# Kernel tuning notes

Measured on AMD Instinct MI355X. Metric: run time of the kernel, lower is better.

## Reference

```python
import jax, jax.numpy as jnp
import numpy as np

DIM = 1024
NUM_HEADS = 16
HEAD_DIM = DIM // NUM_HEADS
EPS = 1e-6


def layer_norm(x, gamma, beta):
    # normalize over last dim (head_dim)
    mu = jnp.mean(x, axis=-1, keepdims=True)
    var = jnp.mean(jnp.square(x - mu), axis=-1, keepdims=True)
    return (x - mu) / jnp.sqrt(var + EPS) * gamma + beta


def apply_rope(q, k):
    # q, k: [B, S, H, D]; computed in fp32 (attn_fp32=True)
    seq_len, head_dim = q.shape[1], q.shape[3]
    half = head_dim // 2
    freq_range = jnp.arange(half, dtype=jnp.float32) / half
    inv_freq = 1.0 / (10000.0 ** freq_range)                       # [half]
    t = jnp.arange(seq_len, dtype=jnp.float32)                     # [S]
    freqs = jnp.outer(t, inv_freq)                                 # [S, half]
    emb = jnp.concatenate([freqs, freqs], axis=-1)                 # [S, D]
    cos = jnp.cos(emb)[None, :, None, :]                           # [1, S, 1, D]
    sin = jnp.sin(emb)[None, :, None, :]

    def rotate_half(x):
        x1, x2 = x[..., :half], x[..., half:]
        return jnp.concatenate([-x2, x1], axis=-1)

    return q * cos + rotate_half(q) * sin, k * cos + rotate_half(k) * sin


def setup_inputs() -> dict:
    key = jax.random.key(0)
    ks = jax.random.split(key, 4)
    B, S = 2, 2048
    x = jax.random.normal(ks[0], (B, S, DIM), dtype=jnp.float32)
    # xavier-uniform-ish scale for linear weights (torch Linear layout: [out, in])
    lim_qkv = float(np.sqrt(6.0 / (DIM + 3 * DIM)))
    w_qkv = jax.random.uniform(ks[1], (3 * DIM, DIM), dtype=jnp.float32, minval=-lim_qkv, maxval=lim_qkv)
    lim_p = float(np.sqrt(6.0 / (DIM + DIM)))
    w_proj = jax.random.uniform(ks[2], (DIM, DIM), dtype=jnp.float32, minval=-lim_p, maxval=lim_p)
    b_proj = jnp.zeros((DIM,), dtype=jnp.float32)
    q_gamma = jnp.ones((HEAD_DIM,), dtype=jnp.float32)
    q_beta = jnp.zeros((HEAD_DIM,), dtype=jnp.float32)
    k_gamma = jnp.ones((HEAD_DIM,), dtype=jnp.float32)
    k_beta = jnp.zeros((HEAD_DIM,), dtype=jnp.float32)
    return {"x": x, "w_qkv": w_qkv, "w_proj": w_proj, "b_proj": b_proj,
            "q_gamma": q_gamma, "q_beta": q_beta, "k_gamma": k_gamma, "k_beta": k_beta}


def reference(x, w_qkv, w_proj, b_proj, q_gamma, q_beta, k_gamma, k_beta):
    B, S, C = x.shape
    H, D = NUM_HEADS, HEAD_DIM
    qkv = jnp.einsum('bsc,oc->bso', x, w_qkv).reshape(B, S, 3, H, D)
    q = layer_norm(qkv[:, :, 0], q_gamma, q_beta)   # [B, S, H, D]
    k = layer_norm(qkv[:, :, 1], k_gamma, k_beta)
    v = qkv[:, :, 2]
    q, k = apply_rope(q, k)
    # attn_fp32=True: scores in fp32
    scale = D ** (-0.5)
    q = q.astype(jnp.float32) * scale
    k = k.astype(jnp.float32)
    v = v.astype(jnp.float32)
    attn = jnp.einsum('bqhd,bkhd->bhqk', q, k)      # [B, H, S, S]
    attn = jax.nn.softmax(attn, axis=-1)
    out = jnp.einsum('bhqk,bkhd->bqhd', attn, v).reshape(B, S, C)
    out = jnp.einsum('bsc,oc->bso', out, w_proj) + b_proj
    return out
```

## Files before the change

### kernel.cpp

```cpp
#include <hip/hip_runtime.h>
#include <math.h>

#define DIM   1024
#define NH    16
#define HD    64
#define BATCH 2
#define SEQ   2048
#define EPS   1e-6f

typedef __attribute__((ext_vector_type(8))) short bf16x8;
typedef __attribute__((ext_vector_type(4))) float f32x4;

#define EXP2F(x) __builtin_amdgcn_exp2f(x)
#define LOG2E 1.4426950408889634f
#define SOFTMAX_SHIFT 12.0f

__device__ __forceinline__ float bf2f(unsigned short u) {
  return __uint_as_float(((unsigned int)u) << 16);
}
__device__ __forceinline__ unsigned short f2bf(float f) {
  unsigned int u = __float_as_uint(f);
  unsigned int r = (u + 0x7FFFu + ((u >> 16) & 1u)) >> 16;
  return (unsigned short)r;
}
__device__ __forceinline__ unsigned int pack_bf16_trunc(float p0, float p1) {
  return (__float_as_uint(p1) & 0xFFFF0000u) | (__float_as_uint(p0) >> 16);
}

__device__ __forceinline__ void async_copy16(const void* g, void* l) {
  __builtin_amdgcn_global_load_lds(
      (const __attribute__((address_space(1))) unsigned int*)g,
      (__attribute__((address_space(3))) unsigned int*)l, 16, 0, 0);
}


__global__ void detect_dtype(const unsigned short* __restrict__ w, int* __restrict__ flag) {
  __shared__ int cnt;
  if (threadIdx.x == 0) cnt = 0;
  __syncthreads();
  int c = 0;
  for (int i = threadIdx.x; i < 4096; i += 256) {
    unsigned short u = w[i];
    if ((u & 0x7F80u) >= 0x3F80u) ++c;
  }
  atomicAdd(&cnt, c);
  __syncthreads();
  if (threadIdx.x == 0) *flag = (cnt >= 64) ? 1 : 0;
}

__global__ __launch_bounds__(256)
void rope_table(float2* __restrict__ tab) {
  const int idx = blockIdx.x * 256 + threadIdx.x;
  const int s = idx >> 5, f = idx & 31;
  const float invf = expf(-((float)f * (1.f / 32.f)) * 9.210340371976184f);
  float sn, cs;
  sincosf((float)s * invf, &sn, &cs);
  tab[idx] = make_float2(cs, sn);
}

__global__ __launch_bounds__(256)
void convert_bf16(const void* __restrict__ src, unsigned short* __restrict__ dst,
                  int n, const int* __restrict__ flagp) {
  const bool isf32 = (*flagp != 0);
  const int i = (blockIdx.x * 256 + threadIdx.x) * 8;
  if (i >= n) return;
  if (isf32) {
    const float* s = (const float*)src + i;
    float4 a = *(const float4*)s;
    float4 b = *(const float4*)(s + 4);
    ushort4 lo, hi;
    lo.x = f2bf(a.x); lo.y = f2bf(a.y); lo.z = f2bf(a.z); lo.w = f2bf(a.w);
    hi.x = f2bf(b.x); hi.y = f2bf(b.y); hi.z = f2bf(b.z); hi.w = f2bf(b.w);
    *(ushort4*)&dst[i] = lo;
    *(ushort4*)&dst[i + 4] = hi;
  } else {
    *(uint4*)&dst[i] = *(const uint4*)((const unsigned short*)src + i);
  }
}

__device__ __forceinline__ float ld_param(const void* p, bool isf32, int idx) {
  return isf32 ? ((const float*)p)[idx] : bf2f(((const unsigned short*)p)[idx]);
}

__global__ __launch_bounds__(256)
void gemm_qkv(const unsigned short* __restrict__ A, const unsigned short* __restrict__ B,
              unsigned short* __restrict__ Qb, unsigned short* __restrict__ Kb,
              unsigned short* __restrict__ VbT,
              const void* __restrict__ qg, const void* __restrict__ qbe,
              const void* __restrict__ kg, const void* __restrict__ kbe,
              const float2* __restrict__ tab, const int* __restrict__ flagp) {
  __shared__ __attribute__((aligned(16))) unsigned short As[128 * 32];
  __shared__ __attribute__((aligned(16))) unsigned short Bs[128 * 32];

  const int K = DIM;
  const int tid  = threadIdx.x;
  const int wv   = tid >> 6;
  const int lane = tid & 63;
  const int l15  = lane & 15;
  const int quad = lane >> 4;
  const int wm = wv >> 1, wn = wv & 1;
  const int bm = blockIdx.y * 128;
  const int bn = blockIdx.x * 128;
  const int qsw = (quad ^ ((l15 >> 1) & 3)) * 8;

  f32x4 acc[4][4];
#pragma unroll
  for (int i = 0; i < 4; ++i)
#pragma unroll
    for (int j = 0; j < 4; ++j) acc[i][j] = (f32x4){0.f, 0.f, 0.f, 0.f};

  const int srow = tid >> 2;
  const int kseg = (((tid & 3) ^ ((tid >> 3) & 3))) * 8;
  const unsigned short* Ag = A + (size_t)(bm + srow) * K + kseg;
  const unsigned short* Bg = B + (size_t)(bn + srow) * K + kseg;
  unsigned short* AsW = &As[wv * 512];
  unsigned short* BsW = &Bs[wv * 512];

  for (int k0 = 0; k0 < K; k0 += 32) {
    __syncthreads();
    async_copy16(Ag + k0, AsW);
    async_copy16(Ag + (size_t)64 * K + k0, AsW + 2048);
    async_copy16(Bg + k0, BsW);
    async_copy16(Bg + (size_t)64 * K + k0, BsW + 2048);
    __syncthreads();

    bf16x8 af[4], bf[4];
#pragma unroll
    for (int mt = 0; mt < 4; ++mt)
      af[mt] = *(const bf16x8*)&As[(wm * 64 + mt * 16 + l15) * 32 + qsw];
#pragma unroll
    for (int nt = 0; nt < 4; ++nt)
      bf[nt] = *(const bf16x8*)&Bs[(wn * 64 + nt * 16 + l15) * 32 + qsw];
#pragma unroll
    for (int mt = 0; mt < 4; ++mt)
#pragma unroll
      for (int nt = 0; nt < 4; ++nt)
        acc[mt][nt] = __builtin_amdgcn_mfma_f32_16x16x32_bf16(af[mt], bf[nt], acc[mt][nt], 0, 0, 0);
  }

  const bool isf32 = (*flagp != 0);
  const int type = bn >> 10;
  const int h = ((bn & 1023) >> 6) + wn;

  if (type == 2) {
#pragma unroll
    for (int mt = 0; mt < 4; ++mt) {
      const int r0 = bm + wm * 64 + mt * 16 + quad * 4;
      const int b = r0 >> 11, s0 = r0 & 2047;
#pragma unroll
      for (int nt = 0; nt < 4; ++nt) {
        const int d = nt * 16 + l15;
        uint2 pk;
        pk.x = ((unsigned int)f2bf(acc[mt][nt][1]) << 16) | f2bf(acc[mt][nt][0]);
        pk.y = ((unsigned int)f2bf(acc[mt][nt][3]) << 16) | f2bf(acc[mt][nt][2]);
        *(uint2*)&VbT[((size_t)(b * NH + h) * HD + d) * SEQ + s0] = pk;
      }
    }
    return;
  }

  unsigned short* plane = (type == 0) ? Qb : Kb;
  const void* gp = (type == 0) ? qg : kg;
  const void* bp = (type == 0) ? qbe : kbe;
  float gam[4], bet[4];
#pragma unroll
  for (int nt = 0; nt < 4; ++nt) {
    gam[nt] = ld_param(gp, isf32, nt * 16 + l15);
    bet[nt] = ld_param(bp, isf32, nt * 16 + l15);
  }
  const float scale = (type == 0) ? (0.125f * LOG2E) : 1.f;

#pragma unroll
  for (int mt = 0; mt < 4; ++mt)
#pragma unroll
    for (int rr = 0; rr < 4; ++rr) {
      const int r = bm + wm * 64 + mt * 16 + quad * 4 + rr;
      const int b = r >> 11, s = r & 2047;
      float sum = acc[mt][0][rr] + acc[mt][1][rr] + acc[mt][2][rr] + acc[mt][3][rr];
      sum += __shfl_xor(sum, 1); sum += __shfl_xor(sum, 2);
      sum += __shfl_xor(sum, 4); sum += __shfl_xor(sum, 8);
      const float mu = sum * (1.f / 64.f);
      float vs = 0.f;
#pragma unroll
      for (int nt = 0; nt < 4; ++nt) {
        const float d = acc[mt][nt][rr] - mu;
        vs += d * d;
      }
      vs += __shfl_xor(vs, 1); vs += __shfl_xor(vs, 2);
      vs += __shfl_xor(vs, 4); vs += __shfl_xor(vs, 8);
      const float rs = rsqrtf(vs * (1.f / 64.f) + EPS);
      float xn[4];
#pragma unroll
      for (int nt = 0; nt < 4; ++nt)
        xn[nt] = (acc[mt][nt][rr] - mu) * rs * gam[nt] + bet[nt];
      const float2 t0 = tab[s * 32 + l15];
      const float2 t1 = tab[s * 32 + 16 + l15];
      float ro[4];
      ro[0] = xn[0] * t0.x - xn[2] * t0.y;
      ro[2] = xn[2] * t0.x + xn[0] * t0.y;
      ro[1] = xn[1] * t1.x - xn[3] * t1.y;
      ro[3] = xn[3] * t1.x + xn[1] * t1.y;
      unsigned short* row = plane + (((size_t)(b * NH + h) * SEQ + s) * HD);
#pragma unroll
      for (int nt = 0; nt < 4; ++nt)
        row[nt * 16 + l15] = f2bf(ro[nt] * scale);
    }
}

#define KIDX(g,k0,key,dim) (((((g)*2+(k0))*64+(key))*32)+(dim))
#define VOFF 8192
#define POFF 16384
#define PIDX(w,row,col) (POFF + ((w)*32+(row))*72 + (col))

__global__ __launch_bounds__(512, 4)
void attn_mfma5(const unsigned short* __restrict__ Qb, const unsigned short* __restrict__ Kb,
                const unsigned short* __restrict__ VbT, unsigned short* __restrict__ O) {
  __shared__ __attribute__((aligned(16))) unsigned short SMEM[34816];

  const int tid  = threadIdx.x;
  const int wv   = tid >> 6;
  const int g    = wv >> 2;
  const int qsub = wv & 3;
  const int lane = tid & 63;
  const int l15  = lane & 15;
  const int quad = lane >> 4;
  const int bh = blockIdx.y;
  const int q0 = blockIdx.x * 128;
  const size_t base  = (size_t)bh * (SEQ * HD);
  const size_t baseT = (size_t)bh * (HD * SEQ);
  const int qsw = (quad ^ ((l15 >> 1) & 3)) * 8;

  bf16x8 qf[2][2];
#pragma unroll
  for (int mt = 0; mt < 2; ++mt)
#pragma unroll
    for (int k0 = 0; k0 < 2; ++k0)
      qf[mt][k0] = *(const bf16x8*)&Qb[base + (size_t)(q0 + qsub * 32 + mt * 16 + l15) * HD + k0 * 32 + quad * 8];

  bf16x8 ones;
#pragma unroll
  for (int j = 0; j < 8; ++j) ones[j] = (short)0x3F80;

  f32x4 oaccT[4][2];
  f32x4 ol[2];
#pragma unroll
  for (int nb = 0; nb < 4; ++nb)
#pragma unroll
    for (int mt = 0; mt < 2; ++mt) oaccT[nb][mt] = (f32x4){0.f, 0.f, 0.f, 0.f};
  ol[0] = (f32x4){0.f, 0.f, 0.f, 0.f};
  ol[1] = (f32x4){0.f, 0.f, 0.f, 0.f};

  const int sseg = (((lane & 3) ^ ((lane >> 3) & 3))) * 8;
  const unsigned short* srcK = Kb + base + (size_t)(qsub * 16 + (lane >> 2)) * HD + sseg;
  const unsigned short* srcV = VbT + baseT + (size_t)(qsub * 16 + (lane >> 2)) * SEQ + sseg;
  unsigned short* dstK0 = &SMEM[KIDX(g, 0, qsub * 16, 0)];
  unsigned short* dstK1 = &SMEM[KIDX(g, 1, qsub * 16, 0)];
  unsigned short* dstV0 = &SMEM[VOFF + KIDX(g, 0, qsub * 16, 0)];
  unsigned short* dstV1 = &SMEM[VOFF + KIDX(g, 1, qsub * 16, 0)];

  for (int it = 0; it < SEQ / 128; ++it) {
    const int kt = it * 128 + g * 64;
    __syncthreads();
    async_copy16(srcK + (size_t)kt * HD,      dstK0);
    async_copy16(srcK + (size_t)kt * HD + 32, dstK1);
    async_copy16(srcV + kt,                   dstV0);
    async_copy16(srcV + kt + 32,              dstV1);
    __syncthreads();

    f32x4 st[4][2];
#pragma unroll
    for (int nb = 0; nb < 4; ++nb)
#pragma unroll
      for (int mt = 0; mt < 2; ++mt) st[nb][mt] = (f32x4){0.f, 0.f, 0.f, 0.f};
#pragma unroll
    for (int k0 = 0; k0 < 2; ++k0)
#pragma unroll
      for (int nb = 0; nb < 4; ++nb) {
        bf16x8 kf = *(const bf16x8*)&SMEM[KIDX(g, k0, nb * 16 + l15, qsw)];
#pragma unroll
        for (int mt = 0; mt < 2; ++mt)
          st[nb][mt] = __builtin_amdgcn_mfma_f32_16x16x32_bf16(kf, qf[mt][k0], st[nb][mt], 0, 0, 0);
      }

#pragma unroll
    for (int mt = 0; mt < 2; ++mt)
#pragma unroll
      for (int nb = 0; nb < 4; ++nb) {
        const float p0 = EXP2F(st[nb][mt][0] - SOFTMAX_SHIFT);
        const float p1 = EXP2F(st[nb][mt][1] - SOFTMAX_SHIFT);
        const float p2 = EXP2F(st[nb][mt][2] - SOFTMAX_SHIFT);
        const float p3 = EXP2F(st[nb][mt][3] - SOFTMAX_SHIFT);
        uint2 pk;
        pk.x = pack_bf16_trunc(p0, p1);
        pk.y = pack_bf16_trunc(p2, p3);
        *(uint2*)&SMEM[PIDX(wv, mt * 16 + l15, nb * 16 + quad * 4)] = pk;
      }

#pragma unroll
    for (int k0 = 0; k0 < 2; ++k0) {
      bf16x8 pf0 = *(const bf16x8*)&SMEM[PIDX(wv, 0 * 16 + l15, k0 * 32 + quad * 8)];
      bf16x8 pf1 = *(const bf16x8*)&SMEM[PIDX(wv, 1 * 16 + l15, k0 * 32 + quad * 8)];
      ol[0] = __builtin_amdgcn_mfma_f32_16x16x32_bf16(ones, pf0, ol[0], 0, 0, 0);
      ol[1] = __builtin_amdgcn_mfma_f32_16x16x32_bf16(ones, pf1, ol[1], 0, 0, 0);
#pragma unroll
      for (int nb = 0; nb < 4; ++nb) {
        bf16x8 vf = *(const bf16x8*)&SMEM[VOFF + KIDX(g, k0, nb * 16 + l15, qsw)];
        oaccT[nb][0] = __builtin_amdgcn_mfma_f32_16x16x32_bf16(vf, pf0, oaccT[nb][0], 0, 0, 0);
        oaccT[nb][1] = __builtin_amdgcn_mfma_f32_16x16x32_bf16(vf, pf1, oaccT[nb][1], 0, 0, 0);
      }
    }
  }

  __syncthreads();
  f32x4* MO = (f32x4*)SMEM;
  float* ML = (float*)(SMEM + POFF);
  if (g == 1) {
#pragma unroll
    for (int mt = 0; mt < 2; ++mt) {
#pragma unroll
      for (int nb = 0; nb < 4; ++nb)
        MO[(((qsub * 2 + mt) * 4 + nb) << 6) + lane] = oaccT[nb][mt];
      if (quad == 0)
        ML[(qsub * 2 + mt) * 16 + l15] = ol[mt][0];
    }
  }
  __syncthreads();
  if (g == 0) {
    const int b = bh >> 4, h = bh & 15;
#pragma unroll
    for (int mt = 0; mt < 2; ++mt) {
      const float l1 = ML[(qsub * 2 + mt) * 16 + l15];
      const float inv = 1.f / (ol[mt][0] + l1);
      const int qrow = q0 + qsub * 32 + mt * 16 + l15;
      unsigned short* orow = O + ((size_t)(b * SEQ + qrow)) * DIM + h * HD;
#pragma unroll
      for (int nb = 0; nb < 4; ++nb) {
        f32x4 o1 = MO[(((qsub * 2 + mt) * 4 + nb) << 6) + lane];
        uint2 pk;
        pk.x = ((unsigned int)f2bf((oaccT[nb][mt][1] + o1[1]) * inv) << 16) |
               f2bf((oaccT[nb][mt][0] + o1[0]) * inv);
        pk.y = ((unsigned int)f2bf((oaccT[nb][mt][3] + o1[3]) * inv) << 16) |
               f2bf((oaccT[nb][mt][2] + o1[2]) * inv);
        *(uint2*)&orow[nb * 16 + quad * 4] = pk;
      }
    }
  }
}

__global__ __launch_bounds__(256)
void gemm_out(const unsigned short* __restrict__ A, const unsigned short* __restrict__ B,
              const void* __restrict__ biasv, void* __restrict__ Cv,
              int M, int N, int K, const int* __restrict__ flagp) {
  __shared__ __attribute__((aligned(16))) unsigned short As[128 * 32];
  __shared__ __attribute__((aligned(16))) unsigned short Bs[64 * 32];

  const int tid  = threadIdx.x;
  const int wv   = tid >> 6;
  const int lane = tid & 63;
  const int l15  = lane & 15;
  const int quad = lane >> 4;
  const int wm = wv >> 1, wn = wv & 1;
  const int bm = blockIdx.y * 128;
  const int bn = blockIdx.x * 64;
  const int qsw = (quad ^ ((l15 >> 1) & 3)) * 8;

  f32x4 acc[4][2];
#pragma unroll
  for (int i = 0; i < 4; ++i)
#pragma unroll
    for (int j = 0; j < 2; ++j) acc[i][j] = (f32x4){0.f, 0.f, 0.f, 0.f};

  const int srow = tid >> 2;
  const int kseg = (((tid & 3) ^ ((tid >> 3) & 3))) * 8;
  const unsigned short* Ag = A + (size_t)(bm + srow) * K + kseg;
  const unsigned short* Bg = B + (size_t)(bn + srow) * K + kseg;
  unsigned short* AsW = &As[wv * 512];
  unsigned short* BsW = &Bs[wv * 512];

  for (int k0 = 0; k0 < K; k0 += 32) {
    __syncthreads();
    async_copy16(Ag + k0, AsW);
    async_copy16(Ag + (size_t)64 * K + k0, AsW + 2048);
    async_copy16(Bg + k0, BsW);
    __syncthreads();

    bf16x8 af[4], bf[2];
#pragma unroll
    for (int mt = 0; mt < 4; ++mt)
      af[mt] = *(const bf16x8*)&As[(wm * 64 + mt * 16 + l15) * 32 + qsw];
#pragma unroll
    for (int nt = 0; nt < 2; ++nt)
      bf[nt] = *(const bf16x8*)&Bs[(wn * 32 + nt * 16 + l15) * 32 + qsw];
#pragma unroll
    for (int mt = 0; mt < 4; ++mt)
#pragma unroll
      for (int nt = 0; nt < 2; ++nt)
        acc[mt][nt] = __builtin_amdgcn_mfma_f32_16x16x32_bf16(af[mt], bf[nt], acc[mt][nt], 0, 0, 0);
  }

  const bool isf32 = (*flagp != 0);
#pragma unroll
  for (int mt = 0; mt < 4; ++mt)
#pragma unroll
    for (int rr = 0; rr < 4; ++rr) {
      const int r = bm + wm * 64 + mt * 16 + quad * 4 + rr;
#pragma unroll
      for (int nt = 0; nt < 2; ++nt) {
        const int c = bn + wn * 32 + nt * 16 + l15;
        const float bias_c = isf32 ? ((const float*)biasv)[c]
                                   : bf2f(((const unsigned short*)biasv)[c]);
        const float o = acc[mt][nt][rr] + bias_c;
        if (isf32) ((float*)Cv)[(size_t)r * N + c] = o;
        else       ((unsigned short*)Cv)[(size_t)r * N + c] = f2bf(o);
      }
    }
}

extern "C" void kernel_launch(void* const* d_in, const int* in_sizes, int n_in,
                              void* d_out, int out_size, void* d_ws, size_t ws_size,
                              hipStream_t stream) {
  const void* x      = d_in[0];
  const void* w_qkv  = d_in[1];
  const void* w_proj = d_in[2];
  const void* b_proj = d_in[3];
  const void* q_g    = d_in[4];
  const void* q_b    = d_in[5];
  const void* k_g    = d_in[6];
  const void* k_b    = d_in[7];

  const size_t PLANE = (size_t)BATCH * NH * SEQ * HD;
  const int NX = BATCH * SEQ * DIM;
  const int NWQ = 3 * DIM * DIM;
  const int NWP = DIM * DIM;

  unsigned short* Qb  = (unsigned short*)d_ws;
  unsigned short* Kb  = Qb + PLANE;
  unsigned short* VbT = Kb + PLANE;
  unsigned short* xb  = VbT + PLANE;
  unsigned short* wqb = xb + PLANE;
  unsigned short* wpb = wqb + NWQ;
  float2* tab = (float2*)(wpb + NWP);
  int* flag = (int*)(tab + SEQ * 32);

  hipLaunchKernelGGL(detect_dtype, dim3(1), dim3(256), 0, stream,
                     (const unsigned short*)w_qkv, flag);
  hipLaunchKernelGGL(rope_table, dim3(SEQ * 32 / 256), dim3(256), 0, stream, tab);

  hipLaunchKernelGGL(convert_bf16, dim3(NX / 8 / 256), dim3(256), 0, stream,
                     x, xb, NX, flag);
  hipLaunchKernelGGL(convert_bf16, dim3(NWQ / 8 / 256), dim3(256), 0, stream,
                     w_qkv, wqb, NWQ, flag);
  hipLaunchKernelGGL(convert_bf16, dim3(NWP / 8 / 256), dim3(256), 0, stream,
                     w_proj, wpb, NWP, flag);

  {
    dim3 grid((3 * DIM) / 128, (BATCH * SEQ) / 128);
    hipLaunchKernelGGL(gemm_qkv, grid, dim3(256), 0, stream,
                       xb, wqb, Qb, Kb, VbT, q_g, q_b, k_g, k_b, tab, flag);
  }
  {
    dim3 grid(SEQ / 128, BATCH * NH);
    hipLaunchKernelGGL(attn_mfma5, grid, dim3(512), 0, stream,
                       Qb, Kb, VbT, xb);
  }
  {
    dim3 grid(DIM / 64, (BATCH * SEQ) / 128);
    hipLaunchKernelGGL(gemm_out, grid, dim3(256), 0, stream,
                       xb, wpb, b_proj, d_out, BATCH * SEQ, DIM, DIM, flag);
  }
}
```

Before: 220.1 us.

## Double-buffer LDS tiles in GEMMs and merge three conversion launches into one

Both GEMM kernels (QKV and output projection) now keep two LDS buffers. The next K-tile's async copies are issued before the MFMAs on the current tile, and one barrier per iteration replaces the previous two, so global loads overlap with compute. Separately, the three bf16 conversion launches are merged into a single kernel that picks its source and destination from the flat index, saving two launches. The cost is double the LDS use in the GEMMs, which may lower occupancy. Whether the asynchronous copies have actually landed before the barrier depends on how async_copy16 waits.

```diff
diff --git a/kernel.cpp b/kernel.cpp
--- a/kernel.cpp
+++ b/kernel.cpp
@@ -7,6 +7,10 @@
 #define BATCH 2
 #define SEQ   2048
 #define EPS   1e-6f
+
+#define NX  (BATCH * SEQ * DIM)
+#define NWQ (3 * DIM * DIM)
+#define NWP (DIM * DIM)
 
 typedef __attribute__((ext_vector_type(8))) short bf16x8;
 typedef __attribute__((ext_vector_type(4))) float f32x4;
@@ -59,11 +63,18 @@
 }
 
 __global__ __launch_bounds__(256)
-void convert_bf16(const void* __restrict__ src, unsigned short* __restrict__ dst,
-                  int n, const int* __restrict__ flagp) {
+void convert_all(const void* __restrict__ x, const void* __restrict__ wq,
+                 const void* __restrict__ wp,
+                 unsigned short* __restrict__ xb, unsigned short* __restrict__ wqb,
+                 unsigned short* __restrict__ wpb, const int* __restrict__ flagp) {
   const bool isf32 = (*flagp != 0);
-  const int i = (blockIdx.x * 256 + threadIdx.x) * 8;
-  if (i >= n) return;
+  int i = (blockIdx.x * 256 + threadIdx.x) * 8;
+  const void* src;
+  unsigned short* dst;
+  if (i < NX) { src = x; dst = xb; }
+  else if (i < NX + NWQ) { src = wq; dst = wqb; i -= NX; }
+  else if (i < NX + NWQ + NWP) { src = wp; dst = wpb; i -= NX + NWQ; }
+  else return;
   if (isf32) {
     const float* s = (const float*)src + i;
     float4 a = *(const float4*)s;
@@ -89,8 +100,8 @@
               const void* __restrict__ qg, const void* __restrict__ qbe,
               const void* __restrict__ kg, const void* __restrict__ kbe,
               const float2* __restrict__ tab, const int* __restrict__ flagp) {
-  __shared__ __attribute__((aligned(16))) unsigned short As[128 * 32];
-  __shared__ __attribute__((aligned(16))) unsigned short Bs[128 * 32];
+  __shared__ __attribute__((aligned(16))) unsigned short As[2][128 * 32];
+  __shared__ __attribute__((aligned(16))) unsigned short Bs[2][128 * 32];
 
   const int K = DIM;
   const int tid  = threadIdx.x;
@@ -113,29 +124,35 @@
   const int kseg = (((tid & 3) ^ ((tid >> 3) & 3))) * 8;
   const unsigned short* Ag = A + (size_t)(bm + srow) * K + kseg;
   const unsigned short* Bg = B + (size_t)(bn + srow) * K + kseg;
-  unsigned short* AsW = &As[wv * 512];
-  unsigned short* BsW = &Bs[wv * 512];
+
+  async_copy16(Ag, &As[0][wv * 512]);
+  async_copy16(Ag + (size_t)64 * K, &As[0][wv * 512 + 2048]);
+  async_copy16(Bg, &Bs[0][wv * 512]);
+  async_copy16(Bg + (size_t)64 * K, &Bs[0][wv * 512 + 2048]);
+  __syncthreads();
 
   for (int k0 = 0; k0 < K; k0 += 32) {
-    __syncthreads();
-    async_copy16(Ag + k0, AsW);
-    async_copy16(Ag + (size_t)64 * K + k0, AsW + 2048);
-    async_copy16(Bg + k0, BsW);
-    async_copy16(Bg + (size_t)64 * K + k0, BsW + 2048);
-    __syncthreads();
+    const int cur = (k0 >> 5) & 1, nxt = cur ^ 1;
+    if (k0 + 32 < K) {
+      async_copy16(Ag + k0 + 32, &As[nxt][wv * 512]);
+      async_copy16(Ag + (size_t)64 * K + k0 + 32, &As[nxt][wv * 512 + 2048]);
+      async_copy16(Bg + k0 + 32, &Bs[nxt][wv * 512]);
+      async_copy16(Bg + (size_t)64 * K + k0 + 32, &Bs[nxt][wv * 512 + 2048]);
+    }
 
     bf16x8 af[4], bf[4];
 #pragma unroll
     for (int mt = 0; mt < 4; ++mt)
-      af[mt] = *(const bf16x8*)&As[(wm * 64 + mt * 16 + l15) * 32 + qsw];
+      af[mt] = *(const bf16x8*)&As[cur][(wm * 64 + mt * 16 + l15) * 32 + qsw];
 #pragma unroll
     for (int nt = 0; nt < 4; ++nt)
-      bf[nt] = *(const bf16x8*)&Bs[(wn * 64 + nt * 16 + l15) * 32 + qsw];
+      bf[nt] = *(const bf16x8*)&Bs[cur][(wn * 64 + nt * 16 + l15) * 32 + qsw];
 #pragma unroll
     for (int mt = 0; mt < 4; ++mt)
 #pragma unroll
       for (int nt = 0; nt < 4; ++nt)
         acc[mt][nt] = __builtin_amdgcn_mfma_f32_16x16x32_bf16(af[mt], bf[nt], acc[mt][nt], 0, 0, 0);
+    __syncthreads();
   }
 
   const bool isf32 = (*flagp != 0);
@@ -351,8 +368,8 @@
 void gemm_out(const unsigned short* __restrict__ A, const unsigned short* __restrict__ B,
               const void* __restrict__ biasv, void* __restrict__ Cv,
               int M, int N, int K, const int* __restrict__ flagp) {
-  __shared__ __attribute__((aligned(16))) unsigned short As[128 * 32];
-  __shared__ __attribute__((aligned(16))) unsigned short Bs[64 * 32];
+  __shared__ __attribute__((aligned(16))) unsigned short As[2][128 * 32];
+  __shared__ __attribute__((aligned(16))) unsigned short Bs[2][64 * 32];
 
   const int tid  = threadIdx.x;
   const int wv   = tid >> 6;
@@ -374,28 +391,33 @@
   const int kseg = (((tid & 3) ^ ((tid >> 3) & 3))) * 8;
   const unsigned short* Ag = A + (size_t)(bm + srow) * K + kseg;
   const unsigned short* Bg = B + (size_t)(bn + srow) * K + kseg;
-  unsigned short* AsW = &As[wv * 512];
-  unsigned short* BsW = &Bs[wv * 512];
+
+  async_copy16(Ag, &As[0][wv * 512]);
+  async_copy16(Ag + (size_t)64 * K, &As[0][wv * 512 + 2048]);
+  async_copy16(Bg, &Bs[0][wv * 512]);
+  __syncthreads();
 
   for (int k0 = 0; k0 < K; k0 += 32) {
-    __syncthreads();
-    async_copy16(Ag + k0, AsW);
-    async_copy16(Ag + (size_t)64 * K + k0, AsW + 2048);
-    async_copy16(Bg + k0, BsW);
-    __syncthreads();
+    const int cur = (k0 >> 5) & 1, nxt = cur ^ 1;
+    if (k0 + 32 < K) {
+      async_copy16(Ag + k0 + 32, &As[nxt][wv * 512]);
+      async_copy16(Ag + (size_t)64 * K + k0 + 32, &As[nxt][wv * 512 + 2048]);
+      async_copy16(Bg + k0 + 32, &Bs[nxt][wv * 512]);
+    }
 
     bf16x8 af[4], bf[2];
 #pragma unroll
     for (int mt = 0; mt < 4; ++mt)
-      af[mt] = *(const bf16x8*)&As[(wm * 64 + mt * 16 + l15) * 32 + qsw];
+      af[mt] = *(const bf16x8*)&As[cur][(wm * 64 + mt * 16 + l15) * 32 + qsw];
 #pragma unroll
     for (int nt = 0; nt < 2; ++nt)
-      bf[nt] = *(const bf16x8*)&Bs[(wn * 32 + nt * 16 + l15) * 32 + qsw];
+      bf[nt] = *(const bf16x8*)&Bs[cur][(wn * 32 + nt * 16 + l15) * 32 + qsw];
 #pragma unroll
     for (int mt = 0; mt < 4; ++mt)
 #pragma unroll
       for (int nt = 0; nt < 2; ++nt)
         acc[mt][nt] = __builtin_amdgcn_mfma_f32_16x16x32_bf16(af[mt], bf[nt], acc[mt][nt], 0, 0, 0);
+    __syncthreads();
   }
 
   const bool isf32 = (*flagp != 0);
@@ -429,9 +451,6 @@
   const void* k_b    = d_in[7];
 
   const size_t PLANE = (size_t)BATCH * NH * SEQ * HD;
-  const int NX = BATCH * SEQ * DIM;
-  const int NWQ = 3 * DIM * DIM;
-  const int NWP = DIM * DIM;
 
   unsigned short* Qb  = (unsigned short*)d_ws;
   unsigned short* Kb  = Qb + PLANE;
@@ -445,13 +464,8 @@
   hipLaunchKernelGGL(detect_dtype, dim3(1), dim3(256), 0, stream,
                      (const unsigned short*)w_qkv, flag);
   hipLaunchKernelGGL(rope_table, dim3(SEQ * 32 / 256), dim3(256), 0, stream, tab);
-
-  hipLaunchKernelGGL(convert_bf16, dim3(NX / 8 / 256), dim3(256), 0, stream,
-                     x, xb, NX, flag);
-  hipLaunchKernelGGL(convert_bf16, dim3(NWQ / 8 / 256), dim3(256), 0, stream,
-                     w_qkv, wqb, NWQ, flag);
-  hipLaunchKernelGGL(convert_bf16, dim3(NWP / 8 / 256), dim3(256), 0, stream,
-                     w_proj, wpb, NWP, flag);
+  hipLaunchKernelGGL(convert_all, dim3((NX + NWQ + NWP) / 8 / 256), dim3(256), 0, stream,
+                     x, w_qkv, w_proj, xb, wqb, wpb, flag);
 
   {
     dim3 grid((3 * DIM) / 128, (BATCH * SEQ) / 128);
```

Measured after the change: 220.9 us. About the same (+0.4%).
